# Kernel optimization log

Hardware: AMD Instinct MI355X
Metric: run time of the kernel (lower is better)

The kernel has to match this reference:

```python
import jax, jax.numpy as jnp
from jax import lax
import numpy as np

B, DIM, H, W = 8, 192, 128, 128
HEADS = 4


def setup_inputs() -> dict:
    key = jax.random.key(0)
    k1, k2, k3, k4 = jax.random.split(key, 4)
    x = jax.random.normal(k1, (B, DIM, H, W), dtype=jnp.float32)
    w_qkv = jax.random.normal(k2, (2 * DIM, DIM), dtype=jnp.float32) * 0.05
    w_dw = jax.random.normal(k3, (2 * DIM, 1, 3, 3), dtype=jnp.float32) * 0.1
    w_proj = jax.random.normal(k4, (DIM, DIM), dtype=jnp.float32) * 0.05
    temperature = jnp.ones((HEADS, 1, 1), dtype=jnp.float32)
    return {"x": x, "w_qkv": w_qkv, "w_dw": w_dw, "w_proj": w_proj, "temperature": temperature}


def reference(x, w_qkv, w_dw, w_proj, temperature):
    b, c, h, w = x.shape
    heads = temperature.shape[0]
    head_c = c // heads
    # 1x1 conv: dim -> 2*dim
    qkv = jnp.einsum('oc,bchw->bohw', w_qkv, x)
    # 3x3 depthwise conv over 2*dim channels
    qkv = lax.conv_general_dilated(
        qkv, w_dw, window_strides=(1, 1), padding='SAME',
        feature_group_count=2 * c,
        dimension_numbers=('NCHW', 'OIHW', 'NCHW'))
    q, v = jnp.split(qkv, 2, axis=1)
    # [b, heads, head_c, h*w]
    q = q.reshape(b, heads, head_c, h * w)
    v = v.reshape(b, heads, head_c, h * w)
    # L2-normalize q over spatial dim; k = q
    q = q / jnp.linalg.norm(q, axis=-1, keepdims=True)
    # channel-wise attention: [b, heads, head_c, head_c]
    attn = jnp.einsum('bhcn,bhdn->bhcd', q, q) * temperature[None]
    attn = jax.nn.softmax(attn, axis=-1)
    out = jnp.einsum('bhcd,bhdn->bhcn', attn, v)
    out = out.reshape(b, c, h, w)
    # 1x1 projection
    return jnp.einsum('oc,bchw->bohw', w_proj, out)
```

## Files before the change

kernel.cpp:

```cpp
#include <hip/hip_runtime.h>

#define BB 8
#define CC 192
#define C2 384
#define HH 128
#define WW 128
#define NN 16384
#define NHEADS 4
#define HC 48
#define LTK 196
#define LTK2 98

typedef float f32x4 __attribute__((ext_vector_type(4)));
typedef float f32x16 __attribute__((ext_vector_type(16)));
typedef short s16x4 __attribute__((ext_vector_type(4)));
typedef short s16x8 __attribute__((ext_vector_type(8)));
typedef unsigned short u16;
typedef u16 u16x4 __attribute__((ext_vector_type(4)));
typedef u16 u16x8 __attribute__((ext_vector_type(8)));
typedef unsigned int u32;

__device__ __forceinline__ float bfu2f(u32 u16v) {
  return __uint_as_float(u16v << 16);
}
__device__ __forceinline__ u16 f2bfu(float f) {
  u32 u = __float_as_uint(f);
  return (u16)((u + 0x7fffu + ((u >> 16) & 1u)) >> 16);
}
__device__ __forceinline__ s16x8 ldpair(const u16* p) {
  s16x4 lo = *reinterpret_cast<const s16x4*>(p);
  s16x4 hi = *reinterpret_cast<const s16x4*>(p + 16);
  return __builtin_shufflevector(lo, hi, 0, 1, 2, 3, 4, 5, 6, 7);
}
__device__ __forceinline__ s16x8 ldb64pair(const u32* p) {
  s16x4 lo = *reinterpret_cast<const s16x4*>(p);
  s16x4 hi = *reinterpret_cast<const s16x4*>(p + 2);
  return __builtin_shufflevector(lo, hi, 0, 1, 2, 3, 4, 5, 6, 7);
}

__global__ __launch_bounds__(256) void k0_wcvt(const float* __restrict__ w,
                                               u16* __restrict__ wbf) {
  const int i = (blockIdx.x * 256 + threadIdx.x) * 4;
  f32x4 v = *reinterpret_cast<const f32x4*>(&w[i]);
  u16x4 o;
  o[0] = f2bfu(v[0]); o[1] = f2bfu(v[1]); o[2] = f2bfu(v[2]); o[3] = f2bfu(v[3]);
  *reinterpret_cast<u16x4*>(&wbf[i]) = o;
}

__global__ __launch_bounds__(512, 4) void k1_qkv(
    const float* __restrict__ x, const u16* __restrict__ wbf,
    u16* __restrict__ qkv) {
  const int n0 = blockIdx.x * 128;
  const int b  = blockIdx.y;
  __shared__ u16 Xs[128 * LTK];
  u32* Xsw = reinterpret_cast<u32*>(Xs);
  const int t = threadIdx.x, lane = t & 63;
  const int wid = t >> 6, wo = wid >> 1, wn = wid & 1;
  const int l31 = lane & 31, g2 = lane >> 5;

  {
    const int nq = t & 31, cr = t >> 5;
    const int kpb = cr >> 1;
    const int jb = (cr & 1) << 1;
    const float* xb = x + (size_t)b * CC * NN + n0 + 4 * nq;
    #pragma unroll 4
    for (int i = 0; i < 12; ++i) {
      f32x4 v = *reinterpret_cast<const f32x4*>(xb + (size_t)(cr + 16 * i) * NN);
      u32 A  = (u32)f2bfu(v[0]) | ((u32)f2bfu(v[1]) << 16);
      u32 Bp = (u32)f2bfu(v[2]) | ((u32)f2bfu(v[3]) << 16);
      u32 oA = __shfl_xor(A, 32);
      u32 oB = __shfl_xor(Bp, 32);
      u32 va, vb;
      if (cr & 1) {
        va = (oB & 0xffffu) | (Bp << 16);
        vb = (oB >> 16) | (Bp & 0xffff0000u);
      } else {
        va = (A & 0xffffu) | (oA << 16);
        vb = (A >> 16) | (oA & 0xffff0000u);
      }
      const int col = kpb + 8 * i;
      Xsw[(4 * nq + jb) * LTK2 + col] = va;
      Xsw[(4 * nq + jb + 1) * LTK2 + col] = vb;
    }
  }
  __syncthreads();

  const int nbase = wn * 64;
  const u32* brow0 = &Xsw[(nbase + l31) * LTK2 + 4 * g2];
  const u32* brow1 = &Xsw[(nbase + 32 + l31) * LTK2 + 4 * g2];

  for (int ot = 0; ot < 3; ++ot) {
    const int o0 = ot * 128;
    const u16* wr = wbf + (size_t)(o0 + wo * 32 + l31) * CC + 8 * g2;
    f32x16 acc0, acc1;
    #pragma unroll
    for (int e = 0; e < 16; ++e) { acc0[e] = 0.f; acc1[e] = 0.f; }

    s16x8 af0 = *reinterpret_cast<const s16x8*>(wr);
    s16x8 af1 = *reinterpret_cast<const s16x8*>(wr + 16);
    #pragma unroll
    for (int s = 0; s < 6; ++s) {
      s16x8 an0, an1;
      if (s < 5) {
        an0 = *reinterpret_cast<const s16x8*>(wr + (s + 1) * 32);
        an1 = *reinterpret_cast<const s16x8*>(wr + (s + 1) * 32 + 16);
      }
      s16x8 bf00 = ldb64pair(brow0 + 16 * s);
      s16x8 bf01 = ldb64pair(brow0 + 16 * s + 8);
      s16x8 bf10 = ldb64pair(brow1 + 16 * s);
      s16x8 bf11 = ldb64pair(brow1 + 16 * s + 8);
      acc0 = __builtin_amdgcn_mfma_f32_32x32x16_bf16(af0, bf00, acc0, 0, 0, 0);
      acc1 = __builtin_amdgcn_mfma_f32_32x32x16_bf16(af0, bf10, acc1, 0, 0, 0);
      acc0 = __builtin_amdgcn_mfma_f32_32x32x16_bf16(af1, bf01, acc0, 0, 0, 0);
      acc1 = __builtin_amdgcn_mfma_f32_32x32x16_bf16(af1, bf11, acc1, 0, 0, 0);
      af0 = an0; af1 = an1;
    }
    #pragma unroll
    for (int r = 0; r < 16; ++r) {
      const int row = (r & 3) + 8 * (r >> 2) + 4 * g2;
      u16* qp = qkv + ((size_t)b * C2 + o0 + wo * 32 + row) * NN + n0 + nbase + l31;
      qp[0]  = f2bfu(acc0[r]);
      qp[32] = f2bfu(acc1[r]);
    }
  }
}

__global__ __launch_bounds__(256) void k2_dw(
    const u16* __restrict__ qkv, const float* __restrict__ wdw,
    u16* __restrict__ out) {
  const int gid = blockIdx.x;
  const int rb = gid & 7;
  const int plane = gid >> 3;
  const int ch = plane % C2;
  const int t = threadIdx.x;
  const int row = rb * 16 + (t >> 4);
  const int x0 = (t & 15) * 8;
  const u16* p = qkv + (size_t)plane * NN;
  const float* wv = wdw + ch * 9;
  float o[8];
  #pragma unroll
  for (int j = 0; j < 8; ++j) o[j] = 0.f;
  #pragma unroll
  for (int dy = 0; dy < 3; ++dy) {
    const int yy = row + dy - 1;
    if ((unsigned)yy < (unsigned)HH) {
      const u16* rp = p + yy * WW;
      u16x8 m = *reinterpret_cast<const u16x8*>(&rp[x0]);
      float px[10];
      px[0] = (x0 > 0) ? bfu2f(rp[x0 - 1]) : 0.f;
      px[9] = (x0 < 120) ? bfu2f(rp[x0 + 8]) : 0.f;
      #pragma unroll
      for (int j = 0; j < 8; ++j) px[j + 1] = bfu2f(m[j]);
      const float w0 = wv[dy * 3 + 0], w1 = wv[dy * 3 + 1], w2 = wv[dy * 3 + 2];
      #pragma unroll
      for (int j = 0; j < 8; ++j)
        o[j] += w0 * px[j] + w1 * px[j + 1] + w2 * px[j + 2];
    }
  }
  u16x8 ov;
  #pragma unroll
  for (int j = 0; j < 8; ++j) ov[j] = f2bfu(o[j]);
  *reinterpret_cast<u16x8*>(&out[(size_t)plane * NN + row * WW + x0]) = ov;
}

__global__ __launch_bounds__(256) void k3_gram(
    const u16* __restrict__ qkvd, float* __restrict__ gpart) {
  const int bh = blockIdx.x, b = bh >> 2, h = bh & 3;
  const int chunk = blockIdx.y;
  const int t = threadIdx.x, lane = t & 63, wv = t >> 6;
  const int l15 = lane & 15, g = lane >> 4;
  __shared__ float red[4][2304];
  const u16* qb = qkvd + ((size_t)b * C2 + h * HC) * NN;

  f32x4 acc[3][3];
  #pragma unroll
  for (int i = 0; i < 3; ++i)
    #pragma unroll
    for (int j = 0; j < 3; ++j)
      #pragma unroll
      for (int e = 0; e < 4; ++e) acc[i][j][e] = 0.f;

  const int nbase = chunk * 1024 + wv * 256;
  #pragma unroll 2
  for (int st = 0; st < 8; ++st) {
    const int n = nbase + st * 32;
    s16x8 cf[3];
    #pragma unroll
    for (int i = 0; i < 3; ++i)
      cf[i] = ldpair(qb + (size_t)(i * 16 + l15) * NN + n + 4 * g);
    #pragma unroll
    for (int i = 0; i < 3; ++i)
      #pragma unroll
      for (int j = 0; j < 3; ++j)
        acc[i][j] = __builtin_amdgcn_mfma_f32_16x16x32_bf16(cf[i], cf[j], acc[i][j], 0, 0, 0);
  }
  #pragma unroll
  for (int i = 0; i < 3; ++i)
    #pragma unroll
    for (int j = 0; j < 3; ++j)
      #pragma unroll
      for (int r = 0; r < 4; ++r)
        red[wv][(i * 16 + 4 * g + r) * 48 + j * 16 + l15] = acc[i][j][r];
  __syncthreads();
  float* gp = gpart + ((size_t)bh * 16 + chunk) * 2304;
  for (int idx = t; idx < 2304; idx += 256)
    gp[idx] = red[0][idx] + red[1][idx] + red[2][idx] + red[3][idx];
}

__global__ __launch_bounds__(256) void k4_soft(
    const float* __restrict__ gpart, const float* __restrict__ temp,
    float* __restrict__ attn) {
  const int bh = blockIdx.x;
  const int h = bh & 3;
  const int t = threadIdx.x;
  __shared__ float G[2304];
  __shared__ float rn[48];
  for (int idx = t; idx < 2304; idx += 256) {
    float s = 0.f;
    #pragma unroll
    for (int c = 0; c < 16; ++c) s += gpart[((size_t)bh * 16 + c) * 2304 + idx];
    G[idx] = s;
  }
  __syncthreads();
  if (t < 48) rn[t] = rsqrtf(G[t * 48 + t]);
  __syncthreads();
  if (t < 48) {
    const float tm = temp[h];
    float v[48];
    float mx = -1e30f;
    #pragma unroll
    for (int j = 0; j < 48; ++j) {
      v[j] = G[t * 48 + j] * rn[t] * rn[j] * tm;
      mx = fmaxf(mx, v[j]);
    }
    float s = 0.f;
    #pragma unroll
    for (int j = 0; j < 48; ++j) { v[j] = expf(v[j] - mx); s += v[j]; }
    const float inv = 1.f / s;
    #pragma unroll
    for (int j = 0; j < 48; ++j)
      attn[(size_t)bh * 2304 + t * 48 + j] = v[j] * inv;
  }
}

__global__ __launch_bounds__(192) void k5_M(
    const float* __restrict__ wproj, const float* __restrict__ attn,
    u16* __restrict__ Mbf) {
  const int o = blockIdx.x;
  const int b = blockIdx.y;
  const int d = threadIdx.x;
  const int h = d / HC, dl = d % HC;
  const float* wrow = wproj + o * CC + h * HC;
  const float* at = attn + ((size_t)(b * NHEADS + h)) * 2304;
  float s = 0.f;
  #pragma unroll
  for (int c = 0; c < HC; ++c) s = fmaf(wrow[c], at[c * HC + dl], s);
  Mbf[((size_t)b * CC + o) * CC + d] = f2bfu(s);
}

__global__ __launch_bounds__(512, 4) void k6_out(
    const u16* __restrict__ Mbf, const u16* __restrict__ qkvd,
    float* __restrict__ out) {
  const int n0 = blockIdx.x * 128;
  const int b  = blockIdx.y;
  __shared__ u16 Vs[128 * LTK];
  u32* Vsw = reinterpret_cast<u32*>(Vs);
  const int t = threadIdx.x, lane = t & 63;
  const int wid = t >> 6, wo = wid >> 2, wn = wid & 3;
  const int l31 = lane & 31, g2 = lane >> 5;

  {
    const int nq = t & 31, cr = t >> 5;
    const int kpb = cr >> 1;
    const int jb = (cr & 1) << 1;
    const u16* vbp = qkvd + ((size_t)b * C2 + CC) * NN + n0 + 4 * nq;
    #pragma unroll 4
    for (int i = 0; i < 12; ++i) {
      u16x4 m = *reinterpret_cast<const u16x4*>(vbp + (size_t)(cr + 16 * i) * NN);
      u32 A  = (u32)m[0] | ((u32)m[1] << 16);
      u32 Bp = (u32)m[2] | ((u32)m[3] << 16);
      u32 oA = __shfl_xor(A, 32);
      u32 oB = __shfl_xor(Bp, 32);
      u32 va, vb;
      if (cr & 1) {
        va = (oB & 0xffffu) | (Bp << 16);
        vb = (oB >> 16) | (Bp & 0xffff0000u);
      } else {
        va = (A & 0xffffu) | (oA << 16);
        vb = (A >> 16) | (oA & 0xffff0000u);
      }
      const int col = kpb + 8 * i;
      Vsw[(4 * nq + jb) * LTK2 + col] = va;
      Vsw[(4 * nq + jb + 1) * LTK2 + col] = vb;
    }
  }
  __syncthreads();

  const int nloc = wn * 32 + l31;
  const u32* brow = &Vsw[nloc * LTK2 + 4 * g2];
  const u16* Ab = Mbf + (size_t)b * CC * CC;

  for (int ot = 0; ot < 3; ++ot) {
    const int o0 = ot * 64;
    const u16* ar = Ab + (size_t)(o0 + wo * 32 + l31) * CC + 8 * g2;
    f32x16 accA, accB;
    #pragma unroll
    for (int e = 0; e < 16; ++e) { accA[e] = 0.f; accB[e] = 0.f; }

    s16x8 af0 = *reinterpret_cast<const s16x8*>(ar);
    s16x8 af1 = *reinterpret_cast<const s16x8*>(ar + 16);
    #pragma unroll
    for (int s = 0; s < 6; ++s) {
      s16x8 an0, an1;
      if (s < 5) {
        an0 = *reinterpret_cast<const s16x8*>(ar + (s + 1) * 32);
        an1 = *reinterpret_cast<const s16x8*>(ar + (s + 1) * 32 + 16);
      }
      s16x8 bf0 = ldb64pair(brow + 16 * s);
      s16x8 bf1 = ldb64pair(brow + 16 * s + 8);
      accA = __builtin_amdgcn_mfma_f32_32x32x16_bf16(af0, bf0, accA, 0, 0, 0);
      accB = __builtin_amdgcn_mfma_f32_32x32x16_bf16(af1, bf1, accB, 0, 0, 0);
      af0 = an0; af1 = an1;
    }
    #pragma unroll
    for (int r = 0; r < 16; ++r) {
      const int row = (r & 3) + 8 * (r >> 2) + 4 * g2;
      out[((size_t)b * CC + o0 + wo * 32 + row) * NN + n0 + nloc] = accA[r] + accB[r];
    }
  }
}

extern "C" void kernel_launch(void* const* d_in, const int* in_sizes, int n_in,
                              void* d_out, int out_size, void* d_ws, size_t ws_size,
                              hipStream_t stream) {
  const float* x      = (const float*)d_in[0];
  const float* w_qkv  = (const float*)d_in[1];
  const float* w_dw   = (const float*)d_in[2];
  const float* w_proj = (const float*)d_in[3];
  const float* temp   = (const float*)d_in[4];
  float* out = (float*)d_out;

  const size_t OFF_QKV   = 0;
  const size_t OFF_QKVD  = 100663296ULL;
  const size_t OFF_GPART = 201326592ULL;
  const size_t OFF_ATTN  = 206045184ULL;
  const size_t OFF_M     = 206340096ULL;
  const size_t OFF_WBF   = 206929920ULL;
  const size_t NEEDED    = 207077376ULL;
  if (ws_size < NEEDED) return;

  char* ws = (char*)d_ws;
  u16* qkv   = (u16*)(ws + OFF_QKV);
  u16* qkvd  = (u16*)(ws + OFF_QKVD);
  float* gpart = (float*)(ws + OFF_GPART);
  float* attn  = (float*)(ws + OFF_ATTN);
  u16* Mbf   = (u16*)(ws + OFF_M);
  u16* wbf   = (u16*)(ws + OFF_WBF);

  k0_wcvt<<<dim3(72), 256, 0, stream>>>(w_qkv, wbf);
  k1_qkv <<<dim3(128, 8), 512, 0, stream>>>(x, wbf, qkv);
  k2_dw  <<<dim3(BB * C2 * 8), 256, 0, stream>>>(qkv, w_dw, qkvd);
  k3_gram<<<dim3(BB * NHEADS, 16), 256, 0, stream>>>(qkvd, gpart);
  k4_soft<<<dim3(BB * NHEADS), 256, 0, stream>>>(gpart, temp, attn);
  k5_M   <<<dim3(CC, BB), 192, 0, stream>>>(w_proj, attn, Mbf);
  k6_out <<<dim3(128, 8), 512, 0, stream>>>(Mbf, qkvd, out);
}
```

Baseline: 236.9 us.

## Permute LDS rows so MFMA outputs store as packed adjacent-column pairs

```diff
diff --git a/kernel.cpp b/kernel.cpp
--- a/kernel.cpp
+++ b/kernel.cpp
@@ -61,9 +61,11 @@
   {
     const int nq = t & 31, cr = t >> 5;
     const int kpb = cr >> 1;
-    const int jb = (cr & 1) << 1;
+    const int jh = cr & 1;
+    const int prA = 2 * nq + jh;
+    const int prB = 64 + 2 * nq + jh;
     const float* xb = x + (size_t)b * CC * NN + n0 + 4 * nq;
-    #pragma unroll 4
+    #pragma unroll 6
     for (int i = 0; i < 12; ++i) {
       f32x4 v = *reinterpret_cast<const f32x4*>(xb + (size_t)(cr + 16 * i) * NN);
       u32 A  = (u32)f2bfu(v[0]) | ((u32)f2bfu(v[1]) << 16);
@@ -71,7 +73,7 @@
       u32 oA = __shfl_xor(A, 32);
       u32 oB = __shfl_xor(Bp, 32);
       u32 va, vb;
-      if (cr & 1) {
+      if (jh) {
         va = (oB & 0xffffu) | (Bp << 16);
         vb = (oB >> 16) | (Bp & 0xffff0000u);
       } else {
@@ -79,22 +81,22 @@
         vb = (A >> 16) | (oA & 0xffff0000u);
       }
       const int col = kpb + 8 * i;
-      Xsw[(4 * nq + jb) * LTK2 + col] = va;
-      Xsw[(4 * nq + jb + 1) * LTK2 + col] = vb;
-    }
-  }
-  __syncthreads();
-
-  const int nbase = wn * 64;
-  const u32* brow0 = &Xsw[(nbase + l31) * LTK2 + 4 * g2];
-  const u32* brow1 = &Xsw[(nbase + 32 + l31) * LTK2 + 4 * g2];
+      Xsw[prA * LTK2 + col] = va;
+      Xsw[prB * LTK2 + col] = vb;
+    }
+  }
+  __syncthreads();
+
+  const int nb2 = wn * 32;
+  const u32* browE = &Xsw[(nb2 + l31) * LTK2 + 4 * g2];
+  const u32* browO = &Xsw[(64 + nb2 + l31) * LTK2 + 4 * g2];
 
   for (int ot = 0; ot < 3; ++ot) {
     const int o0 = ot * 128;
     const u16* wr = wbf + (size_t)(o0 + wo * 32 + l31) * CC + 8 * g2;
-    f32x16 acc0, acc1;
-    #pragma unroll
-    for (int e = 0; e < 16; ++e) { acc0[e] = 0.f; acc1[e] = 0.f; }
+    f32x16 accE, accO;
+    #pragma unroll
+    for (int e = 0; e < 16; ++e) { accE[e] = 0.f; accO[e] = 0.f; }
 
     s16x8 af0 = *reinterpret_cast<const s16x8*>(wr);
     s16x8 af1 = *reinterpret_cast<const s16x8*>(wr + 16);
@@ -105,22 +107,22 @@
         an0 = *reinterpret_cast<const s16x8*>(wr + (s + 1) * 32);
         an1 = *reinterpret_cast<const s16x8*>(wr + (s + 1) * 32 + 16);
       }
-      s16x8 bf00 = ldb64pair(brow0 + 16 * s);
-      s16x8 bf01 = ldb64pair(brow0 + 16 * s + 8);
-      s16x8 bf10 = ldb64pair(brow1 + 16 * s);
-      s16x8 bf11 = ldb64pair(brow1 + 16 * s + 8);
-      acc0 = __builtin_amdgcn_mfma_f32_32x32x16_bf16(af0, bf00, acc0, 0, 0, 0);
-      acc1 = __builtin_amdgcn_mfma_f32_32x32x16_bf16(af0, bf10, acc1, 0, 0, 0);
-      acc0 = __builtin_amdgcn_mfma_f32_32x32x16_bf16(af1, bf01, acc0, 0, 0, 0);
-      acc1 = __builtin_amdgcn_mfma_f32_32x32x16_bf16(af1, bf11, acc1, 0, 0, 0);
+      s16x8 bfE0 = ldb64pair(browE + 16 * s);
+      s16x8 bfE1 = ldb64pair(browE + 16 * s + 8);
+      s16x8 bfO0 = ldb64pair(browO + 16 * s);
+      s16x8 bfO1 = ldb64pair(browO + 16 * s + 8);
+      accE = __builtin_amdgcn_mfma_f32_32x32x16_bf16(af0, bfE0, accE, 0, 0, 0);
+      accO = __builtin_amdgcn_mfma_f32_32x32x16_bf16(af0, bfO0, accO, 0, 0, 0);
+      accE = __builtin_amdgcn_mfma_f32_32x32x16_bf16(af1, bfE1, accE, 0, 0, 0);
+      accO = __builtin_amdgcn_mfma_f32_32x32x16_bf16(af1, bfO1, accO, 0, 0, 0);
       af0 = an0; af1 = an1;
     }
     #pragma unroll
     for (int r = 0; r < 16; ++r) {
       const int row = (r & 3) + 8 * (r >> 2) + 4 * g2;
-      u16* qp = qkv + ((size_t)b * C2 + o0 + wo * 32 + row) * NN + n0 + nbase + l31;
-      qp[0]  = f2bfu(acc0[r]);
-      qp[32] = f2bfu(acc1[r]);
+      const u32 pk = (u32)f2bfu(accE[r]) | ((u32)f2bfu(accO[r]) << 16);
+      *reinterpret_cast<u32*>(
+          &qkv[((size_t)b * C2 + o0 + wo * 32 + row) * NN + n0 + wn * 64 + 2 * l31]) = pk;
     }
   }
 }
@@ -258,7 +260,7 @@
   Mbf[((size_t)b * CC + o) * CC + d] = f2bfu(s);
 }
 
-__global__ __launch_bounds__(512, 4) void k6_out(
+__global__ __launch_bounds__(256, 4) void k6_out(
     const u16* __restrict__ Mbf, const u16* __restrict__ qkvd,
     float* __restrict__ out) {
   const int n0 = blockIdx.x * 128;
@@ -266,46 +268,49 @@
   __shared__ u16 Vs[128 * LTK];
   u32* Vsw = reinterpret_cast<u32*>(Vs);
   const int t = threadIdx.x, lane = t & 63;
-  const int wid = t >> 6, wo = wid >> 2, wn = wid & 3;
+  const int wid = t >> 6, wo = wid >> 1, wn = wid & 1;
   const int l31 = lane & 31, g2 = lane >> 5;
 
   {
     const int nq = t & 31, cr = t >> 5;
     const int kpb = cr >> 1;
-    const int jb = (cr & 1) << 1;
+    const int jh = cr & 1;
+    const int prA = 2 * nq + jh;
+    const int prB = 64 + 2 * nq + jh;
     const u16* vbp = qkvd + ((size_t)b * C2 + CC) * NN + n0 + 4 * nq;
-    #pragma unroll 4
-    for (int i = 0; i < 12; ++i) {
-      u16x4 m = *reinterpret_cast<const u16x4*>(vbp + (size_t)(cr + 16 * i) * NN);
+    #pragma unroll 6
+    for (int i = 0; i < 24; ++i) {
+      u16x4 m = *reinterpret_cast<const u16x4*>(vbp + (size_t)(cr + 8 * i) * NN);
       u32 A  = (u32)m[0] | ((u32)m[1] << 16);
       u32 Bp = (u32)m[2] | ((u32)m[3] << 16);
       u32 oA = __shfl_xor(A, 32);
       u32 oB = __shfl_xor(Bp, 32);
       u32 va, vb;
-      if (cr & 1) {
+      if (jh) {
         va = (oB & 0xffffu) | (Bp << 16);
         vb = (oB >> 16) | (Bp & 0xffff0000u);
       } else {
         va = (A & 0xffffu) | (oA << 16);
         vb = (A >> 16) | (oA & 0xffff0000u);
       }
-      const int col = kpb + 8 * i;
-      Vsw[(4 * nq + jb) * LTK2 + col] = va;
-      Vsw[(4 * nq + jb + 1) * LTK2 + col] = vb;
-    }
-  }
-  __syncthreads();
-
-  const int nloc = wn * 32 + l31;
-  const u32* brow = &Vsw[nloc * LTK2 + 4 * g2];
+      const int col = kpb + 4 * i;
+      Vsw[prA * LTK2 + col] = va;
+      Vsw[prB * LTK2 + col] = vb;
+    }
+  }
+  __syncthreads();
+
+  const int nb2 = wn * 32;
+  const u32* browE = &Vsw[(nb2 + l31) * LTK2 + 4 * g2];
+  const u32* browO = &Vsw[(64 + nb2 + l31) * LTK2 + 4 * g2];
   const u16* Ab = Mbf + (size_t)b * CC * CC;
 
   for (int ot = 0; ot < 3; ++ot) {
     const int o0 = ot * 64;
     const u16* ar = Ab + (size_t)(o0 + wo * 32 + l31) * CC + 8 * g2;
-    f32x16 accA, accB;
-    #pragma unroll
-    for (int e = 0; e < 16; ++e) { accA[e] = 0.f; accB[e] = 0.f; }
+    f32x16 accE, accO;
+    #pragma unroll
+    for (int e = 0; e < 16; ++e) { accE[e] = 0.f; accO[e] = 0.f; }
 
     s16x8 af0 = *reinterpret_cast<const s16x8*>(ar);
     s16x8 af1 = *reinterpret_cast<const s16x8*>(ar + 16);
@@ -316,16 +321,24 @@
         an0 = *reinterpret_cast<const s16x8*>(ar + (s + 1) * 32);
         an1 = *reinterpret_cast<const s16x8*>(ar + (s + 1) * 32 + 16);
       }
-      s16x8 bf0 = ldb64pair(brow + 16 * s);
-      s16x8 bf1 = ldb64pair(brow + 16 * s + 8);
-      accA = __builtin_amdgcn_mfma_f32_32x32x16_bf16(af0, bf0, accA, 0, 0, 0);
-      accB = __builtin_amdgcn_mfma_f32_32x32x16_bf16(af1, bf1, accB, 0, 0, 0);
+      s16x8 bfE0 = ldb64pair(browE + 16 * s);
+      s16x8 bfE1 = ldb64pair(browE + 16 * s + 8);
+      s16x8 bfO0 = ldb64pair(browO + 16 * s);
+      s16x8 bfO1 = ldb64pair(browO + 16 * s + 8);
+      accE = __builtin_amdgcn_mfma_f32_32x32x16_bf16(af0, bfE0, accE, 0, 0, 0);
+      accO = __builtin_amdgcn_mfma_f32_32x32x16_bf16(af0, bfO0, accO, 0, 0, 0);
+      accE = __builtin_amdgcn_mfma_f32_32x32x16_bf16(af1, bfE1, accE, 0, 0, 0);
+      accO = __builtin_amdgcn_mfma_f32_32x32x16_bf16(af1, bfO1, accO, 0, 0, 0);
       af0 = an0; af1 = an1;
     }
     #pragma unroll
     for (int r = 0; r < 16; ++r) {
       const int row = (r & 3) + 8 * (r >> 2) + 4 * g2;
-      out[((size_t)b * CC + o0 + wo * 32 + row) * NN + n0 + nloc] = accA[r] + accB[r];
+      float2 st;
+      st.x = accE[r];
+      st.y = accO[r];
+      *reinterpret_cast<float2*>(
+          &out[((size_t)b * CC + o0 + wo * 32 + row) * NN + n0 + wn * 64 + 2 * l31]) = st;
     }
   }
 }
@@ -363,5 +376,5 @@
   k3_gram<<<dim3(BB * NHEADS, 16), 256, 0, stream>>>(qkvd, gpart);
   k4_soft<<<dim3(BB * NHEADS), 256, 0, stream>>>(gpart, temp, attn);
   k5_M   <<<dim3(CC, BB), 192, 0, stream>>>(w_proj, attn, Mbf);
-  k6_out <<<dim3(128, 8), 512, 0, stream>>>(Mbf, qkvd, out);
-}
+  k6_out <<<dim3(128, 8), 256, 0, stream>>>(Mbf, qkvd, out);
+}
```

Result: faster. 213.2 us (-10.0%).
